# Kernel optimization log

Measured on AMD Instinct MI355X. Metric: run time of the kernel, lower is better.

## Reference

```python
import jax, jax.numpy as jnp
import numpy as np

N, E, IN, HID, H, OUT = 50000, 800000, 128, 64, 2, 1
NEG_SLOPE = 0.2


def setup_inputs() -> dict:
    key = jax.random.key(0)
    ks = jax.random.split(key, 12)
    g = lambda k, shape, fi, fo: jax.random.normal(k, shape, jnp.float32) * np.sqrt(2.0 / (fi + fo)).astype(np.float32)
    x = jax.random.normal(ks[0], (N, IN), jnp.float32)
    edge_index = jax.random.randint(ks[1], (2, E), 0, N, jnp.int64)
    HC = H * HID
    W1 = g(ks[2], (HC, IN), IN, HC)
    b1 = jnp.zeros((HC,), jnp.float32)
    att1 = g(ks[3], (1, H, HID), HID, HID)
    W2 = g(ks[4], (HC, HC), HC, HC)
    b2 = jnp.zeros((HC,), jnp.float32)
    att2 = g(ks[5], (1, H, HID), HID, HID)
    Wp1 = g(ks[6], (HID, HC), HC, HID)
    bp1 = jnp.zeros((HID,), jnp.float32)
    Wp2 = g(ks[7], (OUT, HID), HID, OUT)
    bp2 = jnp.zeros((OUT,), jnp.float32)
    return {"x": x, "edge_index": edge_index, "W1": W1, "b1": b1, "att1": att1,
            "W2": W2, "b2": b2, "att2": att2, "Wp1": Wp1, "bp1": bp1, "Wp2": Wp2, "bp2": bp2}


def _segment_softmax(alpha, idx, n):
    # alpha: [E, H]; softmax over edges sharing the same destination node
    m = jax.ops.segment_max(alpha, idx, num_segments=n)
    m = jnp.where(jnp.isfinite(m), m, 0.0)  # empty segments -> -inf guard
    ex = jnp.exp(alpha - m[idx])
    s = jax.ops.segment_sum(ex, idx, num_segments=n)
    return ex / (s[idx] + 1e-16)


def _gatv2(x, edge_index, W, b, att):
    n = x.shape[0]
    h, c = att.shape[1], att.shape[2]
    xw = (x @ W.T + b).reshape(n, h, c)          # shared lin_l == lin_r
    src, dst = edge_index[0], edge_index[1]       # x_j = xw[src], x_i = xw[dst]
    xj = xw[src]                                  # [E, H, C]
    e = jax.nn.leaky_relu(xw[dst] + xj, NEG_SLOPE)
    alpha = jnp.einsum('ehc,ohc->eh', e, att)     # [E, H]
    alpha = _segment_softmax(alpha, dst, n)
    msg = xj * alpha[:, :, None]                  # message uses x_j (not e)
    out = jax.ops.segment_sum(msg, dst, num_segments=n)
    return out.reshape(n, h * c)


def reference(x, edge_index, W1, b1, att1, W2, b2, att2, Wp1, bp1, Wp2, bp2):
    # eval mode: dropout is identity
    h = jax.nn.relu(_gatv2(x, edge_index, W1, b1, att1))
    h = jax.nn.relu(_gatv2(h, edge_index, W2, b2, att2))
    h = h @ Wp1.T + bp1
    h = h @ Wp2.T + bp2
    return jax.nn.sigmoid(h)
```

## Files before the change

### kernel.cpp

```cpp
#include <hip/hip_runtime.h>
#include <math.h>

typedef __attribute__((ext_vector_type(2))) float f32x2;
typedef __attribute__((ext_vector_type(4))) float fx4;
typedef __attribute__((ext_vector_type(8))) short s16x8;

#define EC 64
#define NRR 8
#define RRN 6250


__device__ __forceinline__ unsigned pack_bf2(float lo, float hi){
  unsigned ul = __float_as_uint(lo); ul += 0x7fffu + ((ul>>16)&1u);
  unsigned uh = __float_as_uint(hi); uh += 0x7fffu + ((uh>>16)&1u);
  return (uh & 0xffff0000u) | (ul >> 16);
}


__device__ __forceinline__ void gemm_core(uint4* Wl, const float* __restrict__ X,
    const float* __restrict__ b, unsigned short* __restrict__ Ybf, int nrows, int brow, int t)
{
  int wv = t >> 6, lane = t & 63;
  int r = lane & 15, kb = lane >> 4;
  int row = brow*64 + wv*16 + r;
  const float* xrow = &X[(size_t)min(row, nrows-1)*128];

  fx4 acc[8];
  #pragma unroll
  for(int c=0;c<8;c++) acc[c] = (fx4){0.f,0.f,0.f,0.f};

  #pragma unroll
  for(int kt=0;kt<4;kt++){
    int k0 = kt*32 + kb*8;
    float4 v0 = *(const float4*)&xrow[k0];
    float4 v1 = *(const float4*)&xrow[k0+4];
    float vs[8] = {v0.x,v0.y,v0.z,v0.w,v1.x,v1.y,v1.z,v1.w};
    s16x8 ahi, alo;
    #pragma unroll
    for(int j=0;j<8;j++){
      unsigned u = __float_as_uint(vs[j]);
      unsigned uh = u + 0x7fffu + ((u>>16)&1u);
      unsigned short h = (unsigned short)(uh >> 16);
      float hf = __uint_as_float(((unsigned)h)<<16);
      float lo = vs[j] - hf;
      unsigned ul = __float_as_uint(lo);
      ul += 0x7fffu + ((ul>>16)&1u);
      ahi[j] = (short)h;
      alo[j] = (short)(ul>>16);
    }
    int chunk = kt*4 + kb;
    #pragma unroll
    for(int c=0;c<8;c++){
      uint4 wb = Wl[((c*16 + r)<<4) | (chunk ^ r)];
      s16x8 bb = *(s16x8*)&wb;
      acc[c] = __builtin_amdgcn_mfma_f32_16x16x32_bf16(ahi, bb, acc[c], 0,0,0);
      acc[c] = __builtin_amdgcn_mfma_f32_16x16x32_bf16(alo, bb, acc[c], 0,0,0);
    }
  }

  __syncthreads();
  unsigned short* lds = (unsigned short*)Wl;
  unsigned short* my = lds + wv*2048;
  int colb = lane & 15;
  int rq0 = (lane>>4)*4;
  #pragma unroll
  for(int c=0;c<8;c++){
    int col = c*16 + colb;
    float bias = b[col];
    #pragma unroll
    for(int q=0;q<4;q++){
      unsigned u = __float_as_uint(acc[c][q] + bias);
      u += 0x7fffu + ((u>>16)&1u);
      my[(rq0+q)*128 + col] = (unsigned short)(u>>16);
    }
  }
  const uint4* my4 = (const uint4*)my;
  uint4* Y4 = (uint4*)Ybf;
  #pragma unroll
  for(int rr=0;rr<4;rr++){
    int idx = lane + 64*rr;
    int lrow = idx >> 4, lcol = idx & 15;
    int grow = brow*64 + wv*16 + lrow;
    if(grow < nrows)
      Y4[(size_t)grow*16 + lcol] = my4[idx];
  }
}


__global__ __launch_bounds__(256) void mega_k(
    const float* __restrict__ X, const float* __restrict__ W1, const float* __restrict__ b1,
    unsigned short* __restrict__ XWbf, int nrows, int nGB,
    const int* __restrict__ dst, int E, int CH,
    unsigned short* __restrict__ cnt16, int N,
    const float* __restrict__ W2, unsigned short* __restrict__ W2bf,
    const float* __restrict__ Wp1, const float* __restrict__ bp1,
    const float* __restrict__ Wp2, const float* __restrict__ bp2,
    float* __restrict__ wfold)
{
  __shared__ int smem[8192];
  int b = blockIdx.x;
  int t = threadIdx.x;

  if(b < nGB){
    uint4* Wl = (uint4*)smem;
    #pragma unroll
    for(int i=0;i<8;i++){
      int idx = t + i*256;
      int row = idx >> 4, ch = idx & 15;
      const float* wsrc = &W1[(size_t)row*128 + ch*8];
      float4 va = *(const float4*)&wsrc[0];
      float4 vb = *(const float4*)&wsrc[4];
      uint4 o;
      o.x = pack_bf2(va.x, va.y); o.y = pack_bf2(va.z, va.w);
      o.z = pack_bf2(vb.x, vb.y); o.w = pack_bf2(vb.z, vb.w);
      Wl[(row<<4) | (ch ^ (row & 15))] = o;
    }
    __syncthreads();
    gemm_core(Wl, X, b1, XWbf, nrows, b, t);
    return;
  }
  int hb = b - nGB;
  if(hb < NRR*EC){
    int r = hb >> 6, c = hb & (EC-1);
    int r0 = r*RRN, rend = min(r0+RRN, N);
    int rn = rend - r0;
    if(rn <= 0) return;
    for(int d=t; d<rn; d+=256) smem[d] = 0;
    __syncthreads();
    int e0 = c*CH, e1 = min(e0+CH, E);
    for(int e = e0+t; e < e1; e += 256){
      int d = dst[e];
      if(d >= r0 && d < rend) atomicAdd(&smem[d-r0], 1);
    }
    __syncthreads();
    unsigned short* outp = cnt16 + (size_t)c*N;
    for(int d=t; d<rn; d+=256) outp[r0+d] = (unsigned short)smem[d];
    return;
  }
  int tb = hb - NRR*EC;
  if(tb == 0){
    const float4* Ws = (const float4*)W2;
    uint2* Wd = (uint2*)W2bf;
    #pragma unroll
    for(int i=0;i<16;i++){
      int idx = t + i*256;
      float4 v = Ws[idx];
      uint2 o; o.x = pack_bf2(v.x, v.y); o.y = pack_bf2(v.z, v.w);
      Wd[idx] = o;
    }
    return;
  }
  int k = t;
  if(k < 128){
    float s = 0.f;
    for(int j=0;j<64;j++) s += Wp2[j]*Wp1[(size_t)j*128 + k];
    wfold[k] = s;
  } else if(k == 128){
    float s = bp2[0];
    for(int j=0;j<64;j++) s += Wp2[j]*bp1[j];
    wfold[128] = s;
  }
}


__global__ __launch_bounds__(1024) void scan1_k(const unsigned short* __restrict__ cnt16,
    unsigned short* __restrict__ offs16, int* __restrict__ total,
    int* __restrict__ bsum, int n){
  __shared__ int ws[16];
  int i = blockIdx.x*1024 + threadIdx.x;
  int v = 0;
  if(i < n){
    int s = 0;
    #pragma unroll
    for(int c=0;c<EC;c++){
      int tc = cnt16[(size_t)c*n + i];
      offs16[(size_t)c*n + i] = (unsigned short)s;
      s += tc;
    }
    total[i] = s;
    v = s;
  }
  #pragma unroll
  for(int m=1;m<64;m<<=1) v += __shfl_xor(v, m);
  if((threadIdx.x & 63) == 0) ws[threadIdx.x >> 6] = v;
  __syncthreads();
  if(threadIdx.x == 0){
    int s = 0;
    #pragma unroll
    for(int w=0; w<16; w++) s += ws[w];
    bsum[blockIdx.x] = s;
  }
}

__global__ __launch_bounds__(1024) void scan2_k(int* __restrict__ bsum, int nb,
                                                int* __restrict__ row_ptr, int n, int E){
  __shared__ int sm[1024];
  int t = threadIdx.x;
  int v = (t < nb) ? bsum[t] : 0;
  sm[t] = v;
  __syncthreads();
  for(int off=1; off<1024; off<<=1){
    int tv = (t>=off)? sm[t-off] : 0;
    __syncthreads();
    sm[t] += tv;
    __syncthreads();
  }
  if(t < nb) bsum[t] = sm[t] - v;
  if(t == 0) row_ptr[n] = E;
}

__global__ void scan3_k(const int* __restrict__ total, const int* __restrict__ bsum,
                        int* __restrict__ row_ptr, int n){
  __shared__ int sm[1024];
  int i = blockIdx.x*1024 + threadIdx.x;
  int v = (i<n)? total[i] : 0;
  sm[threadIdx.x] = v;
  __syncthreads();
  for(int off=1; off<1024; off<<=1){
    int t = (threadIdx.x>=off)? sm[threadIdx.x-off] : 0;
    __syncthreads();
    sm[threadIdx.x] += t;
    __syncthreads();
  }
  if(i<n)
    row_ptr[i] = sm[threadIdx.x] - v + bsum[blockIdx.x];
}


__global__ __launch_bounds__(256) void fillC_k(
    const int* __restrict__ src, const int* __restrict__ dst,
    const unsigned short* __restrict__ offs16, const int* __restrict__ row_ptr,
    int* __restrict__ csr_src, int E, int CH, int N)
{
  __shared__ int cursor[RRN];
  int b = blockIdx.x, t = threadIdx.x;
  int r = b >> 6, c = b & (EC-1);
  int r0 = r*RRN, rend = min(r0+RRN, N);
  int rn = rend - r0;
  if(rn <= 0) return;
  for(int d=t; d<rn; d+=256)
    cursor[d] = row_ptr[r0+d] + (int)offs16[(size_t)c*N + r0 + d];
  __syncthreads();
  int e0 = c*CH, e1 = min(e0+CH, E);
  for(int base = e0 + t; base < e1; base += 1024){
    int ea = base, eb = base+256, ec2 = base+512, ed = base+768;
    int da = dst[ea];
    int db = (eb < e1) ? dst[eb] : -1;
    int dc = (ec2 < e1) ? dst[ec2] : -1;
    int dd = (ed < e1) ? dst[ed] : -1;
    int sa = src[ea];
    int sb = (eb < e1) ? src[eb] : 0;
    int sc = (ec2 < e1) ? src[ec2] : 0;
    int sd = (ed < e1) ? src[ed] : 0;
    if(da >= r0 && da < rend){ int p = atomicAdd(&cursor[da-r0], 1); csr_src[p] = sa; }
    if(db >= r0 && db < rend){ int p = atomicAdd(&cursor[db-r0], 1); csr_src[p] = sb; }
    if(dc >= r0 && dc < rend){ int p = atomicAdd(&cursor[dc-r0], 1); csr_src[p] = sc; }
    if(dd >= r0 && dd < rend){ int p = atomicAdd(&cursor[dd-r0], 1); csr_src[p] = sd; }
  }
}


__global__ __launch_bounds__(256) void gemm_mfma_k(
    const float* __restrict__ X, const unsigned short* __restrict__ Wbf,
    const float* __restrict__ b, unsigned short* __restrict__ Ybf, int nrows)
{
  __shared__ uint4 Wl[128*16];
  int t = threadIdx.x;
  {
    const uint4* Ws = (const uint4*)Wbf;
    #pragma unroll
    for(int i=0;i<8;i++){
      int idx = t + i*256;
      int row = idx >> 4, ch = idx & 15;
      Wl[(row<<4) | (ch ^ (row & 15))] = Ws[idx];
    }
  }
  __syncthreads();
  gemm_core(Wl, X, b, Ybf, nrows, blockIdx.x, t);
}


#define BFLO(u) __uint_as_float((u)<<16)
#define BFHI(u) __uint_as_float((u)&0xffff0000u)
#define DPP_ADD(v, ctrl) { int _t = __builtin_amdgcn_update_dpp(0, __float_as_int(v), ctrl, 0xF, 0xF, true); (v) += __int_as_float(_t); }

template<int FUSE>
__global__ __launch_bounds__(256) void gat_v4_k(
    const unsigned short* __restrict__ XWbf,
    const float* __restrict__ att,
    const int* __restrict__ row_ptr, const int* __restrict__ csr_src,
    float* __restrict__ outp, const float* __restrict__ wfold, int n)
{
  int wid = threadIdx.x >> 6, lane = threadIdx.x & 63;
  int node = blockIdx.x*4 + wid;
  if(node >= n) return;
  int g = lane >> 4;
  int cg = lane & 15;
  int c8 = cg * 8;

  float4 A0 = *(const float4*)&att[c8];
  float4 A1 = *(const float4*)&att[c8+4];
  f32x2 a[4] = { {A0.x,A0.y}, {A0.z,A0.w}, {A1.x,A1.y}, {A1.z,A1.w} };

  const uint4* XW4 = (const uint4*)XWbf;
  uint4 du = XW4[(size_t)node*16 + cg];
  f32x2 xd[4] = { {BFLO(du.x),BFHI(du.x)}, {BFLO(du.y),BFHI(du.y)},
                  {BFLO(du.z),BFHI(du.z)}, {BFLO(du.w),BFHI(du.w)} };

  int beg = row_ptr[node], end = row_ptr[node+1];
  float s = 0.f;
  f32x2 acc[4] = {{0.f,0.f},{0.f,0.f},{0.f,0.f},{0.f,0.f}};

  if(end > beg){
    int sn_cur = csr_src[min(beg + g, end-1)];
    int sn_nxt = (beg+4 < end) ? csr_src[min(beg+4 + g, end-1)] : sn_cur;
    uint4 u = XW4[(size_t)sn_cur*16 + cg];
    for(int i = beg; i < end; i += 4){
      uint4 u_nxt = XW4[(size_t)sn_nxt*16 + cg];
      int sn_nn = (i+8 < end) ? csr_src[min(i+8 + g, end-1)] : sn_nxt;
      bool ok = (i + g) < end;

      f32x2 x0 = {BFLO(u.x), BFHI(u.x)};
      f32x2 x1 = {BFLO(u.y), BFHI(u.y)};
      f32x2 x2 = {BFLO(u.z), BFHI(u.z)};
      f32x2 x3 = {BFLO(u.w), BFHI(u.w)};
      f32x2 v0 = xd[0]+x0, v1 = xd[1]+x1, v2 = xd[2]+x2, v3 = xd[3]+x3;
      f32x2 q0 = v0*0.2f, q1 = v1*0.2f, q2 = v2*0.2f, q3 = v3*0.2f;
      f32x2 l0, l1, l2, l3;
      l0.x = fmaxf(v0.x,q0.x); l0.y = fmaxf(v0.y,q0.y);
      l1.x = fmaxf(v1.x,q1.x); l1.y = fmaxf(v1.y,q1.y);
      l2.x = fmaxf(v2.x,q2.x); l2.y = fmaxf(v2.y,q2.y);
      l3.x = fmaxf(v3.x,q3.x); l3.y = fmaxf(v3.y,q3.y);
      f32x2 p2 = l0*a[0];
      p2 += l1*a[1];
      p2 += l2*a[2];
      p2 += l3*a[3];
      float p = p2.x + p2.y;
      DPP_ADD(p, 0xB1);
      DPP_ADD(p, 0x4E);
      DPP_ADD(p, 0x141);
      float ex = ok ? __expf(fminf(p, 60.f)) : 0.f;
      s += ex;
      f32x2 e2 = {ex, ex};
      acc[0] += e2*x0;
      acc[1] += e2*x1;
      acc[2] += e2*x2;
      acc[3] += e2*x3;

      u = u_nxt; sn_nxt = sn_nn;
    }
  }

  s += __shfl_xor(s,16);  s += __shfl_xor(s,32);
  #pragma unroll
  for(int j=0;j<4;j++){
    acc[j].x += __shfl_xor(acc[j].x,16); acc[j].x += __shfl_xor(acc[j].x,32);
    acc[j].y += __shfl_xor(acc[j].y,16); acc[j].y += __shfl_xor(acc[j].y,32);
  }

  float inv = (s > 0.f) ? 1.f/s : 0.f;
  f32x2 o[4];
  #pragma unroll
  for(int j=0;j<4;j++){
    o[j].x = fmaxf(acc[j].x*inv, 0.f);
    o[j].y = fmaxf(acc[j].y*inv, 0.f);
  }

  if(FUSE == 0){
    if(lane < 16){
      *(float4*)&outp[(size_t)node*128 + c8]     = make_float4(o[0].x,o[0].y,o[1].x,o[1].y);
      *(float4*)&outp[(size_t)node*128 + c8 + 4] = make_float4(o[2].x,o[2].y,o[3].x,o[3].y);
    }
  } else {
    float4 wf0 = *(const float4*)&wfold[c8];
    float4 wf1 = *(const float4*)&wfold[c8+4];
    float tt = o[0].x*wf0.x + o[0].y*wf0.y + o[1].x*wf0.z + o[1].y*wf0.w
             + o[2].x*wf1.x + o[2].y*wf1.y + o[3].x*wf1.z + o[3].y*wf1.w;
    DPP_ADD(tt, 0xB1);
    DPP_ADD(tt, 0x4E);
    DPP_ADD(tt, 0x141);
    DPP_ADD(tt, 0x140);
    if(lane == 0)
      outp[node] = 1.f/(1.f + __expf(-(tt + wfold[128])));
  }
}


static inline size_t alignup(size_t v){ return (v + 255) & ~(size_t)255; }

extern "C" void kernel_launch(void* const* d_in, const int* in_sizes, int n_in,
                              void* d_out, int out_size, void* d_ws, size_t ws_size,
                              hipStream_t stream) {
  const float* x    = (const float*)d_in[0];
  const int*   ei   = (const int*)  d_in[1];
  const float* W1   = (const float*)d_in[2];
  const float* b1   = (const float*)d_in[3];
  const float* att1 = (const float*)d_in[4];
  const float* W2   = (const float*)d_in[5];
  const float* b2   = (const float*)d_in[6];
  const float* att2 = (const float*)d_in[7];
  const float* Wp1  = (const float*)d_in[8];
  const float* bp1  = (const float*)d_in[9];
  const float* Wp2  = (const float*)d_in[10];
  const float* bp2  = (const float*)d_in[11];
  float* out = (float*)d_out;

  int N = in_sizes[0] / 128;
  int E = in_sizes[1] / 2;
  int CH = (E + EC - 1) / EC;

  char* ws = (char*)d_ws;
  size_t off = 0;
  float* G1            = (float*)(ws + off); off = alignup(off + (size_t)N*128*sizeof(float));
  unsigned short* XWbf = (unsigned short*)(ws + off); off = alignup(off + (size_t)N*128*sizeof(unsigned short));
  int* csr_src  = (int*)(ws + off); off = alignup(off + (size_t)E*sizeof(int));
  unsigned short* cnt16  = (unsigned short*)(ws + off); off = alignup(off + (size_t)EC*N*sizeof(unsigned short));
  unsigned short* offs16 = (unsigned short*)(ws + off); off = alignup(off + (size_t)EC*N*sizeof(unsigned short));
  int* row_ptr  = (int*)(ws + off); off = alignup(off + (size_t)(N+1)*sizeof(int));
  int* total    = (int*)(ws + off); off = alignup(off + (size_t)N*sizeof(int));
  int* bsum     = (int*)(ws + off); off = alignup(off + 1024*sizeof(int));
  unsigned short* W2bf = (unsigned short*)(ws + off); off = alignup(off + 128*128*sizeof(unsigned short));
  float* wfold  = (float*)(ws + off); off = alignup(off + 129*sizeof(float));

  const int* esrc = ei;
  const int* edst = ei + E;

  int nGB = (N + 63) / 64;
  int nb = (N + 1023) / 1024;

  mega_k<<<nGB + NRR*EC + 2, 256, 0, stream>>>(
      x, W1, b1, XWbf, N, nGB,
      edst, E, CH, cnt16, N,
      W2, W2bf, Wp1, bp1, Wp2, bp2, wfold);

  scan1_k<<<nb, 1024, 0, stream>>>(cnt16, offs16, total, bsum, N);
  scan2_k<<<1, 1024, 0, stream>>>(bsum, nb, row_ptr, N, E);
  scan3_k<<<nb, 1024, 0, stream>>>(total, bsum, row_ptr, N);
  fillC_k<<<NRR*EC, 256, 0, stream>>>(esrc, edst, offs16, row_ptr, csr_src, E, CH, N);

  gat_v4_k<0><<<(N+3)/4, 256, 0, stream>>>(XWbf, att1, row_ptr, csr_src, G1, nullptr, N);
  gemm_mfma_k<<<nGB, 256, 0, stream>>>(G1, W2bf, b2, XWbf, N);
  gat_v4_k<1><<<(N+3)/4, 256, 0, stream>>>(XWbf, att2, row_ptr, csr_src, out, wfold, N);
}
```

Before: 139.1 us.

## Store layer-1 output in bf16, read it in GEMM, merge scan passes

```diff
diff --git a/kernel.cpp b/kernel.cpp
--- a/kernel.cpp
+++ b/kernel.cpp
@@ -192,11 +192,20 @@
   }
 }
 
-__global__ __launch_bounds__(1024) void scan2_k(int* __restrict__ bsum, int nb,
-                                                int* __restrict__ row_ptr, int n, int E){
+
+__global__ __launch_bounds__(1024) void scan3_k(const int* __restrict__ total,
+    const int* __restrict__ bsum, int nb, int* __restrict__ row_ptr, int n){
   __shared__ int sm[1024];
+  __shared__ int base_s;
   int t = threadIdx.x;
-  int v = (t < nb) ? bsum[t] : 0;
+  if(t < 64){
+    int bv = (t < nb && t < (int)blockIdx.x) ? bsum[t] : 0;
+    #pragma unroll
+    for(int m=1;m<64;m<<=1) bv += __shfl_xor(bv, m);
+    if(t == 0) base_s = bv;
+  }
+  int i = blockIdx.x*1024 + t;
+  int v = (i<n)? total[i] : 0;
   sm[t] = v;
   __syncthreads();
   for(int off=1; off<1024; off<<=1){
@@ -205,25 +214,10 @@
     sm[t] += tv;
     __syncthreads();
   }
-  if(t < nb) bsum[t] = sm[t] - v;
-  if(t == 0) row_ptr[n] = E;
-}
-
-__global__ void scan3_k(const int* __restrict__ total, const int* __restrict__ bsum,
-                        int* __restrict__ row_ptr, int n){
-  __shared__ int sm[1024];
-  int i = blockIdx.x*1024 + threadIdx.x;
-  int v = (i<n)? total[i] : 0;
-  sm[threadIdx.x] = v;
-  __syncthreads();
-  for(int off=1; off<1024; off<<=1){
-    int t = (threadIdx.x>=off)? sm[threadIdx.x-off] : 0;
-    __syncthreads();
-    sm[threadIdx.x] += t;
-    __syncthreads();
-  }
-  if(i<n)
-    row_ptr[i] = sm[threadIdx.x] - v + bsum[blockIdx.x];
+  if(i<n){
+    row_ptr[i] = sm[t] - v + base_s;
+    if(i == n-1) row_ptr[n] = sm[t] + base_s;
+  }
 }
 
 
@@ -260,8 +254,8 @@
 }
 
 
-__global__ __launch_bounds__(256) void gemm_mfma_k(
-    const float* __restrict__ X, const unsigned short* __restrict__ Wbf,
+__global__ __launch_bounds__(256) void gemm_bf2_k(
+    const unsigned short* __restrict__ Xbf, const unsigned short* __restrict__ Wbf,
     const float* __restrict__ b, unsigned short* __restrict__ Ybf, int nrows)
 {
   __shared__ uint4 Wl[128*16];
@@ -276,7 +270,55 @@
     }
   }
   __syncthreads();
-  gemm_core(Wl, X, b, Ybf, nrows, blockIdx.x, t);
+
+  int wv = t >> 6, lane = t & 63;
+  int r = lane & 15, kb = lane >> 4;
+  int row = blockIdx.x*64 + wv*16 + r;
+  const uint4* xrow = (const uint4*)&Xbf[(size_t)min(row, nrows-1)*128];
+
+  fx4 acc[8];
+  #pragma unroll
+  for(int c=0;c<8;c++) acc[c] = (fx4){0.f,0.f,0.f,0.f};
+
+  #pragma unroll
+  for(int kt=0;kt<4;kt++){
+    uint4 av = xrow[kt*4 + kb];
+    s16x8 aa = *(s16x8*)&av;
+    int chunk = kt*4 + kb;
+    #pragma unroll
+    for(int c=0;c<8;c++){
+      uint4 wb = Wl[((c*16 + r)<<4) | (chunk ^ r)];
+      s16x8 bb = *(s16x8*)&wb;
+      acc[c] = __builtin_amdgcn_mfma_f32_16x16x32_bf16(aa, bb, acc[c], 0,0,0);
+    }
+  }
+
+  __syncthreads();
+  unsigned short* lds = (unsigned short*)Wl;
+  unsigned short* my = lds + wv*2048;
+  int colb = lane & 15;
+  int rq0 = (lane>>4)*4;
+  #pragma unroll
+  for(int c=0;c<8;c++){
+    int col = c*16 + colb;
+    float bias = b[col];
+    #pragma unroll
+    for(int q=0;q<4;q++){
+      unsigned u = __float_as_uint(acc[c][q] + bias);
+      u += 0x7fffu + ((u>>16)&1u);
+      my[(rq0+q)*128 + col] = (unsigned short)(u>>16);
+    }
+  }
+  const uint4* my4 = (const uint4*)my;
+  uint4* Y4 = (uint4*)Ybf;
+  #pragma unroll
+  for(int rr=0;rr<4;rr++){
+    int idx = lane + 64*rr;
+    int lrow = idx >> 4, lcol = idx & 15;
+    int grow = blockIdx.x*64 + wv*16 + lrow;
+    if(grow < nrows)
+      Y4[(size_t)grow*16 + lcol] = my4[idx];
+  }
 }
 
 
@@ -289,7 +331,8 @@
     const unsigned short* __restrict__ XWbf,
     const float* __restrict__ att,
     const int* __restrict__ row_ptr, const int* __restrict__ csr_src,
-    float* __restrict__ outp, const float* __restrict__ wfold, int n)
+    float* __restrict__ outf, unsigned short* __restrict__ outbf,
+    const float* __restrict__ wfold, int n)
 {
   int wid = threadIdx.x >> 6, lane = threadIdx.x & 63;
   int node = blockIdx.x*4 + wid;
@@ -325,12 +368,10 @@
       f32x2 x2 = {BFLO(u.z), BFHI(u.z)};
       f32x2 x3 = {BFLO(u.w), BFHI(u.w)};
       f32x2 v0 = xd[0]+x0, v1 = xd[1]+x1, v2 = xd[2]+x2, v3 = xd[3]+x3;
-      f32x2 q0 = v0*0.2f, q1 = v1*0.2f, q2 = v2*0.2f, q3 = v3*0.2f;
-      f32x2 l0, l1, l2, l3;
-      l0.x = fmaxf(v0.x,q0.x); l0.y = fmaxf(v0.y,q0.y);
-      l1.x = fmaxf(v1.x,q1.x); l1.y = fmaxf(v1.y,q1.y);
-      l2.x = fmaxf(v2.x,q2.x); l2.y = fmaxf(v2.y,q2.y);
-      l3.x = fmaxf(v3.x,q3.x); l3.y = fmaxf(v3.y,q3.y);
+      f32x2 l0 = __builtin_elementwise_max(v0, v0*0.2f);
+      f32x2 l1 = __builtin_elementwise_max(v1, v1*0.2f);
+      f32x2 l2 = __builtin_elementwise_max(v2, v2*0.2f);
+      f32x2 l3 = __builtin_elementwise_max(v3, v3*0.2f);
       f32x2 p2 = l0*a[0];
       p2 += l1*a[1];
       p2 += l2*a[2];
@@ -368,8 +409,12 @@
 
   if(FUSE == 0){
     if(lane < 16){
-      *(float4*)&outp[(size_t)node*128 + c8]     = make_float4(o[0].x,o[0].y,o[1].x,o[1].y);
-      *(float4*)&outp[(size_t)node*128 + c8 + 4] = make_float4(o[2].x,o[2].y,o[3].x,o[3].y);
+      uint4 o4;
+      o4.x = pack_bf2(o[0].x, o[0].y);
+      o4.y = pack_bf2(o[1].x, o[1].y);
+      o4.z = pack_bf2(o[2].x, o[2].y);
+      o4.w = pack_bf2(o[3].x, o[3].y);
+      *(uint4*)&outbf[(size_t)node*128 + c8] = o4;
     }
   } else {
     float4 wf0 = *(const float4*)&wfold[c8];
@@ -381,7 +426,7 @@
     DPP_ADD(tt, 0x141);
     DPP_ADD(tt, 0x140);
     if(lane == 0)
-      outp[node] = 1.f/(1.f + __expf(-(tt + wfold[128])));
+      outf[node] = 1.f/(1.f + __expf(-(tt + wfold[128])));
   }
 }
 
@@ -411,7 +456,7 @@
 
   char* ws = (char*)d_ws;
   size_t off = 0;
-  float* G1            = (float*)(ws + off); off = alignup(off + (size_t)N*128*sizeof(float));
+  unsigned short* Gbf  = (unsigned short*)(ws + off); off = alignup(off + (size_t)N*128*sizeof(unsigned short));
   unsigned short* XWbf = (unsigned short*)(ws + off); off = alignup(off + (size_t)N*128*sizeof(unsigned short));
   int* csr_src  = (int*)(ws + off); off = alignup(off + (size_t)E*sizeof(int));
   unsigned short* cnt16  = (unsigned short*)(ws + off); off = alignup(off + (size_t)EC*N*sizeof(unsigned short));
@@ -434,11 +479,10 @@
       W2, W2bf, Wp1, bp1, Wp2, bp2, wfold);
 
   scan1_k<<<nb, 1024, 0, stream>>>(cnt16, offs16, total, bsum, N);
-  scan2_k<<<1, 1024, 0, stream>>>(bsum, nb, row_ptr, N, E);
-  scan3_k<<<nb, 1024, 0, stream>>>(total, bsum, row_ptr, N);
+  scan3_k<<<nb, 1024, 0, stream>>>(total, bsum, nb, row_ptr, N);
   fillC_k<<<NRR*EC, 256, 0, stream>>>(esrc, edst, offs16, row_ptr, csr_src, E, CH, N);
 
-  gat_v4_k<0><<<(N+3)/4, 256, 0, stream>>>(XWbf, att1, row_ptr, csr_src, G1, nullptr, N);
-  gemm_mfma_k<<<nGB, 256, 0, stream>>>(G1, W2bf, b2, XWbf, N);
-  gat_v4_k<1><<<(N+3)/4, 256, 0, stream>>>(XWbf, att2, row_ptr, csr_src, out, wfold, N);
-}
+  gat_v4_k<0><<<(N+3)/4, 256, 0, stream>>>(XWbf, att1, row_ptr, csr_src, nullptr, Gbf, nullptr, N);
+  gemm_bf2_k<<<nGB, 256, 0, stream>>>(Gbf, W2bf, b2, XWbf, N);
+  gat_v4_k<1><<<(N+3)/4, 256, 0, stream>>>(XWbf, att2, row_ptr, csr_src, out, nullptr, wfold, N);
+}
```

Result: no change. 138.6 us (-0.3%).
